# Kernel tuning notes

Hardware: AMD Instinct MI355X
Metric: run time of the kernel (lower is better)

Reference implementation:

```python
import jax, jax.numpy as jnp
import numpy as np

DIM = 512   # feature channels (dim)
K = 3       # depthwise kernel size
H = 256     # grid extent along pos[:,0]
W = 256     # grid extent along pos[:,1]
N = 20000   # number of occupied spots (unique coordinates)


def setup_inputs() -> dict:
    key = jax.random.key(0)
    k1, k2, k3 = jax.random.split(key, 3)
    rng = np.random.default_rng(0)
    # N unique flat cells; pin corners so the dense grid extent is exactly HxW
    flat = np.concatenate([[0, H * W - 1], rng.permutation(H * W - 2)[: N - 2] + 1])
    pos = jnp.asarray(np.stack([flat // W, flat % W], axis=1), dtype=jnp.int32)  # (N,2)
    x = jax.random.normal(k1, (1, N, DIM), jnp.float32)
    weight = jax.random.normal(k2, (DIM, 1, K, K), jnp.float32) * 0.05  # depthwise OIHW
    bias = jax.random.normal(k3, (DIM,), jnp.float32) * 0.05
    return {"x": x, "pos": pos, "weight": weight, "bias": bias}


def reference(x, pos, weight, bias):
    pos = pos - pos.min(axis=0)                 # shift to origin (as torch)
    p0, p1 = pos[:, 0], pos[:, 1]
    xsq = x[0]                                  # (N, DIM)
    # scatter sparse coords to dense grid (duplicates would sum, coords unique)
    grid = jnp.zeros((H, W, DIM), x.dtype).at[p0, p1].add(xsq)   # (H, W, DIM)
    xd = grid.transpose(2, 1, 0)[None]          # (1, DIM, W, H) == permute(2,1,0).unsqueeze(0)
    conv = jax.lax.conv_general_dilated(
        xd, weight, (1, 1), "SAME",
        dimension_numbers=("NCHW", "OIHW", "NCHW"),
        feature_group_count=DIM,
    ) + bias[None, :, None, None]
    mask = xd.sum(axis=1, keepdims=True) != 0.0  # occupied cells
    out_d = jnp.where(mask, conv, 0.0) + xd      # masked residual
    dense = out_d[0].transpose(2, 1, 0)          # (H, W, DIM)
    # gather back to sparse values; torch to_sparse(2) orders rows lexicographically
    order = jnp.lexsort((p1, p0))
    vals = dense[p0[order], p1[order]]           # (N, DIM)
    return vals[None]                            # (1, N, DIM)
```

## Files before the change

### kernel.cpp

```cpp
#include <hip/hip_runtime.h>

#define HH 256
#define WW 256
#define DIM 512

typedef float f32x4 __attribute__((ext_vector_type(4)));


__global__ __launch_bounds__(256) void scatter_kernel(const int* __restrict__ pos,
                                                      int* __restrict__ cell_map,
                                                      int n) {
    int i = blockIdx.x * 256 + threadIdx.x;
    if (i >= n) return;
    int p0 = pos[2 * i];
    int p1 = pos[2 * i + 1];
    cell_map[p0 * WW + p1] = i;
}

__global__ __launch_bounds__(256) void rank_kernel(const int* __restrict__ cell_map,
                                                   int* __restrict__ sorted) {
    __shared__ int red[256];
    __shared__ int wt[4];
    const int t = threadIdx.x;
    const int b = blockIdx.x;
    const int limit = b * 256;

    int cnt = 0;
    const int4* cm4 = (const int4*)cell_map;
    for (int i = t; i * 4 < limit; i += 256) {
        int4 v = cm4[i];
        cnt += (v.x >= 0) + (v.y >= 0) + (v.z >= 0) + (v.w >= 0);
    }
    red[t] = cnt;
    __syncthreads();
    #pragma unroll
    for (int d = 128; d > 0; d >>= 1) {
        if (t < d) red[t] += red[t + d];
        __syncthreads();
    }
    int blk_off = red[0];

    int cell = limit + t;
    int m = cell_map[cell];
    bool occ = (m >= 0);
    unsigned long long mask = __ballot(occ);
    int lane = t & 63;
    int wave = t >> 6;
    int pre = __popcll(mask & ((1ull << lane) - 1ull));
    if (lane == 0) wt[wave] = __popcll(mask);
    __syncthreads();
    int woff = 0;
    for (int i = 0; i < wave; ++i) woff += wt[i];
    if (occ) sorted[blk_off + woff + pre] = (m << 16) | cell;
}

__global__ __launch_bounds__(256) void conv_main(const float* __restrict__ x,
                                                 const float* __restrict__ weight,
                                                 const float* __restrict__ bias,
                                                 const int* __restrict__ cell_map,
                                                 const int* __restrict__ sorted,
                                                 float* __restrict__ out,
                                                 int n) {
    const int lane = threadIdx.x & 63;
    const int wv   = threadIdx.x >> 6;
    const int c0   = lane * 8;

    float wtv[72];
    {
        const float4* wb = (const float4*)(weight + c0 * 9);
        #pragma unroll
        for (int q = 0; q < 18; ++q) {
            float4 v = wb[q];
            wtv[4 * q + 0] = v.x; wtv[4 * q + 1] = v.y;
            wtv[4 * q + 2] = v.z; wtv[4 * q + 3] = v.w;
        }
    }
    float bj[8];
    {
        float4 b0 = *(const float4*)(bias + c0);
        float4 b1 = *(const float4*)(bias + c0 + 4);
        bj[0]=b0.x; bj[1]=b0.y; bj[2]=b0.z; bj[3]=b0.w;
        bj[4]=b1.x; bj[5]=b1.y; bj[6]=b1.z; bj[7]=b1.w;
    }
    #pragma unroll
    for (int j = 0; j < 8; ++j) wtv[j * 9 + 4] += 1.0f;

    const int nb  = gridDim.x;
    const int cid = (blockIdx.x & 7) * (nb >> 3) + (blockIdx.x >> 3);
    const int ppb = (n + nb - 1) / nb;
    const int base = cid * ppb;
    int endr = base + ppb; if (endr > n) endr = n;

    int r = base + wv;
    if (r >= endr) return;
    int pk = __builtin_amdgcn_readfirstlane(sorted[r]);

    while (r < endr) {
        const int rn = r + 4;
        int pk_next = 0;
        if (rn < endr)
            pk_next = __builtin_amdgcn_readfirstlane(sorted[rn]);

        const int p    = pk >> 16;
        const int flat = pk & 0xFFFF;
        const int h = flat >> 8;
        const int w = flat & (WW - 1);

        int m[9];
        #pragma unroll
        for (int k = 0; k < 9; ++k) {
            if (k == 4) { m[4] = -1; continue; }
            int dh = k % 3 - 1;
            int dw = k / 3 - 1;
            int hh = h + dh;
            int ww = w + dw;
            int v = -1;
            if ((unsigned)hh < (unsigned)HH && (unsigned)ww < (unsigned)WW)
                v = cell_map[hh * WW + ww];
            m[k] = __builtin_amdgcn_readfirstlane(v);
        }

        const float* xs = x + (size_t)p * DIM + c0;
        float4 s0 = *(const float4*)(xs);
        float4 s1 = *(const float4*)(xs + 4);
        float acc[8];
        acc[0] = bj[0] + s0.x * wtv[0*9+4]; acc[1] = bj[1] + s0.y * wtv[1*9+4];
        acc[2] = bj[2] + s0.z * wtv[2*9+4]; acc[3] = bj[3] + s0.w * wtv[3*9+4];
        acc[4] = bj[4] + s1.x * wtv[4*9+4]; acc[5] = bj[5] + s1.y * wtv[5*9+4];
        acc[6] = bj[6] + s1.z * wtv[6*9+4]; acc[7] = bj[7] + s1.w * wtv[7*9+4];

        #pragma unroll
        for (int k = 0; k < 9; ++k) {
            if (k == 4) continue;
            if (m[k] >= 0) {
                const float* xn = x + (size_t)m[k] * DIM + c0;
                float4 n0 = *(const float4*)(xn);
                float4 n1 = *(const float4*)(xn + 4);
                acc[0] += n0.x * wtv[0*9+k]; acc[1] += n0.y * wtv[1*9+k];
                acc[2] += n0.z * wtv[2*9+k]; acc[3] += n0.w * wtv[3*9+k];
                acc[4] += n1.x * wtv[4*9+k]; acc[5] += n1.y * wtv[5*9+k];
                acc[6] += n1.z * wtv[6*9+k]; acc[7] += n1.w * wtv[7*9+k];
            }
        }

        float* op = out + (size_t)r * DIM + c0;
        f32x4 o0 = { acc[0], acc[1], acc[2], acc[3] };
        f32x4 o1 = { acc[4], acc[5], acc[6], acc[7] };
        __builtin_nontemporal_store(o0, (f32x4*)op);
        __builtin_nontemporal_store(o1, (f32x4*)(op + 4));

        r = rn;
        pk = pk_next;
    }
}

extern "C" void kernel_launch(void* const* d_in, const int* in_sizes, int n_in,
                              void* d_out, int out_size, void* d_ws, size_t ws_size,
                              hipStream_t stream) {
    const float* x      = (const float*)d_in[0];
    const int*   pos    = (const int*)d_in[1];
    const float* weight = (const float*)d_in[2];
    const float* bias   = (const float*)d_in[3];
    float* out = (float*)d_out;

    int n = in_sizes[1] / 2;

    int* ws       = (int*)d_ws;
    int* cell_map = ws;
    int* sorted   = ws + HH * WW;

    scatter_kernel<<<(n + 255) / 256, 256, 0, stream>>>(pos, cell_map, n);
    rank_kernel<<<256, 256, 0, stream>>>(cell_map, sorted);

    const int nblocks = 1024;
    conv_main<<<nblocks, 256, 0, stream>>>(x, weight, bias, cell_map, sorted, out, n);
}
```

Baseline: 123.2 us.

## Split channels across wave pairs and use branchless predicated neighbor loads

Each wave now covers 256 channels with 4 per lane instead of 512 with 8, so two waves share each point and the per-lane weight registers drop from 72 to 36. Neighbor gathers become branchless: missing neighbors load the center row and are multiplied by a zero gate, which lets all nine loads issue together. The grid size doubles to match the smaller work per wave. The cost is more waves reading the cell map and more redundant gather traffic for missing neighbors, in exchange for lower register pressure and more memory-level parallelism.

Result: slower. 132.9 us (+7.9%).

```diff
diff --git a/kernel.cpp b/kernel.cpp
--- a/kernel.cpp
+++ b/kernel.cpp
@@ -63,27 +63,31 @@
                                                  int n) {
     const int lane = threadIdx.x & 63;
     const int wv   = threadIdx.x >> 6;
-    const int c0   = lane * 8;
+    const int c0   = (wv & 1) * 256 + lane * 4;
+    const int eng  = wv >> 1;
 
-    float wtv[72];
+    float wts[36];
     {
+        float wraw[36];
         const float4* wb = (const float4*)(weight + c0 * 9);
         #pragma unroll
-        for (int q = 0; q < 18; ++q) {
+        for (int q = 0; q < 9; ++q) {
             float4 v = wb[q];
-            wtv[4 * q + 0] = v.x; wtv[4 * q + 1] = v.y;
-            wtv[4 * q + 2] = v.z; wtv[4 * q + 3] = v.w;
+            wraw[4*q+0]=v.x; wraw[4*q+1]=v.y; wraw[4*q+2]=v.z; wraw[4*q+3]=v.w;
         }
+        #pragma unroll
+        for (int j = 0; j < 4; ++j)
+            #pragma unroll
+            for (int k = 0; k < 9; ++k)
+                wts[k*4+j] = wraw[j*9+k];
     }
-    float bj[8];
-    {
-        float4 b0 = *(const float4*)(bias + c0);
-        float4 b1 = *(const float4*)(bias + c0 + 4);
-        bj[0]=b0.x; bj[1]=b0.y; bj[2]=b0.z; bj[3]=b0.w;
-        bj[4]=b1.x; bj[5]=b1.y; bj[6]=b1.z; bj[7]=b1.w;
-    }
+    wts[16] += 1.0f; wts[17] += 1.0f; wts[18] += 1.0f; wts[19] += 1.0f;
+    float b0, b1, b2, b3;
+    { float4 bv = *(const float4*)(bias + c0); b0=bv.x; b1=bv.y; b2=bv.z; b3=bv.w; }
+
     #pragma unroll
-    for (int j = 0; j < 8; ++j) wtv[j * 9 + 4] += 1.0f;
+    for (int i = 0; i < 36; ++i) asm volatile("" : "+v"(wts[i]));
+    asm volatile("" : "+v"(b0), "+v"(b1), "+v"(b2), "+v"(b3));
 
     const int nb  = gridDim.x;
     const int cid = (blockIdx.x & 7) * (nb >> 3) + (blockIdx.x >> 3);
@@ -91,12 +95,12 @@
     const int base = cid * ppb;
     int endr = base + ppb; if (endr > n) endr = n;
 
-    int r = base + wv;
+    int r = base + eng;
     if (r >= endr) return;
     int pk = __builtin_amdgcn_readfirstlane(sorted[r]);
 
     while (r < endr) {
-        const int rn = r + 4;
+        const int rn = r + 2;
         int pk_next = 0;
         if (rn < endr)
             pk_next = __builtin_amdgcn_readfirstlane(sorted[rn]);
@@ -106,48 +110,41 @@
         const int h = flat >> 8;
         const int w = flat & (WW - 1);
 
-        int m[9];
+        int   mm[9];
+        float g[9];
         #pragma unroll
         for (int k = 0; k < 9; ++k) {
-            if (k == 4) { m[4] = -1; continue; }
+            if (k == 4) { mm[4] = p; g[4] = 1.0f; continue; }
             int dh = k % 3 - 1;
             int dw = k / 3 - 1;
             int hh = h + dh;
-            int ww = w + dw;
+            int ww2 = w + dw;
             int v = -1;
-            if ((unsigned)hh < (unsigned)HH && (unsigned)ww < (unsigned)WW)
-                v = cell_map[hh * WW + ww];
-            m[k] = __builtin_amdgcn_readfirstlane(v);
+            if ((unsigned)hh < (unsigned)HH && (unsigned)ww2 < (unsigned)WW)
+                v = cell_map[hh * WW + ww2];
+            v = __builtin_amdgcn_readfirstlane(v);
+            g[k]  = (v >= 0) ? 1.0f : 0.0f;
+            mm[k] = (v >= 0) ? v : p;
         }
 
-        const float* xs = x + (size_t)p * DIM + c0;
-        float4 s0 = *(const float4*)(xs);
-        float4 s1 = *(const float4*)(xs + 4);
-        float acc[8];
-        acc[0] = bj[0] + s0.x * wtv[0*9+4]; acc[1] = bj[1] + s0.y * wtv[1*9+4];
-        acc[2] = bj[2] + s0.z * wtv[2*9+4]; acc[3] = bj[3] + s0.w * wtv[3*9+4];
-        acc[4] = bj[4] + s1.x * wtv[4*9+4]; acc[5] = bj[5] + s1.y * wtv[5*9+4];
-        acc[6] = bj[6] + s1.z * wtv[6*9+4]; acc[7] = bj[7] + s1.w * wtv[7*9+4];
+        float4 xv[9];
+        #pragma unroll
+        for (int k = 0; k < 9; ++k)
+            xv[k] = *(const float4*)(x + (size_t)mm[k] * DIM + c0);
 
+        float a0 = b0, a1 = b1, a2 = b2, a3 = b3;
         #pragma unroll
         for (int k = 0; k < 9; ++k) {
-            if (k == 4) continue;
-            if (m[k] >= 0) {
-                const float* xn = x + (size_t)m[k] * DIM + c0;
-                float4 n0 = *(const float4*)(xn);
-                float4 n1 = *(const float4*)(xn + 4);
-                acc[0] += n0.x * wtv[0*9+k]; acc[1] += n0.y * wtv[1*9+k];
-                acc[2] += n0.z * wtv[2*9+k]; acc[3] += n0.w * wtv[3*9+k];
-                acc[4] += n1.x * wtv[4*9+k]; acc[5] += n1.y * wtv[5*9+k];
-                acc[6] += n1.z * wtv[6*9+k]; acc[7] += n1.w * wtv[7*9+k];
-            }
+            float gk = g[k];
+            a0 += xv[k].x * (wts[k*4+0] * gk);
+            a1 += xv[k].y * (wts[k*4+1] * gk);
+            a2 += xv[k].z * (wts[k*4+2] * gk);
+            a3 += xv[k].w * (wts[k*4+3] * gk);
         }
 
         float* op = out + (size_t)r * DIM + c0;
-        f32x4 o0 = { acc[0], acc[1], acc[2], acc[3] };
-        f32x4 o1 = { acc[4], acc[5], acc[6], acc[7] };
-        __builtin_nontemporal_store(o0, (f32x4*)op);
-        __builtin_nontemporal_store(o1, (f32x4*)(op + 4));
+        f32x4 o = { a0, a1, a2, a3 };
+        __builtin_nontemporal_store(o, (f32x4*)op);
 
         r = rn;
         pk = pk_next;
@@ -172,6 +169,6 @@
     scatter_kernel<<<(n + 255) / 256, 256, 0, stream>>>(pos, cell_map, n);
     rank_kernel<<<256, 256, 0, stream>>>(cell_map, sorted);
 
-    const int nblocks = 1024;
+    const int nblocks = 2048;
     conv_main<<<nblocks, 256, 0, stream>>>(x, weight, bias, cell_map, sorted, out, n);
 }
```
